# Kernel optimization log

Hardware: AMD Instinct MI355X
Metric: run time of the kernel (lower is better)

Reference implementation:

```python
import jax, jax.numpy as jnp
import numpy as np

M0, M1 = 32, 16          # multiplicities of 0e (scalars) and 1o (vectors)
FEAT = M0 + 3 * M1       # 80
WNUM = M0*M0 + M1*M1 + M0*M1 + M1*M0  # 2304 per-edge TP weights
N_NODES, N_EDGES, N_RBF, HID = 10000, 160000, 50, 64
EPS = 1e-5
INV_SQRT3 = 1.0 / np.sqrt(3.0)
# per-path normalization: 1/sqrt(num_paths_to_output * mul_in)
A_P1 = 1.0 / np.sqrt(2.0 * M0)   # 0e x 0e -> 0e
A_P4 = 1.0 / np.sqrt(2.0 * M1)   # 1o x 1o -> 0e
A_P2 = 1.0 / np.sqrt(2.0 * M1)   # 1o x 0e -> 1o
A_P3 = 1.0 / np.sqrt(2.0 * M0)   # 0e x 1o -> 1o


def setup_inputs() -> dict:
    key = jax.random.key(0)
    ks = jax.random.split(key, 12)
    def lin(k, fi, fo):
        return jax.random.normal(k, (fi, fo), jnp.float32) / np.sqrt(fi)
    return dict(
        h=jax.random.normal(ks[0], (N_NODES, FEAT), jnp.float32),
        edge_index=jax.random.randint(ks[1], (2, N_EDGES), 0, N_NODES),
        edge_sh=jax.random.normal(ks[2], (N_EDGES, 4), jnp.float32),
        edge_features=jax.random.normal(ks[3], (N_EDGES, N_RBF), jnp.float32),
        W1e=lin(ks[4], N_RBF, HID), b1e=jnp.zeros(HID, jnp.float32),
        W2e=lin(ks[5], HID, HID), b2e=jnp.zeros(HID, jnp.float32),
        W3e=lin(ks[6], HID, WNUM) * 0.1, b3e=jnp.zeros(WNUM, jnp.float32),
        A0=jax.random.normal(ks[7], (M0, M0), jnp.float32),
        A1p=jax.random.normal(ks[8], (M1, M1), jnp.float32),
        bn_w0=jnp.ones(M0, jnp.float32), bn_b0=jnp.zeros(M0, jnp.float32),
        bn_w1=jnp.ones(M1, jnp.float32),
    )


def _forward(h, edge_index, edge_sh, edge_features,
             W1e, b1e, W2e, b2e, W3e, b3e, A0, A1p, bn_w0, bn_b0, bn_w1):
    N = h.shape[0]
    E = edge_sh.shape[0]
    src, dst = edge_index[0], edge_index[1]

    # ---- edge MLP -> per-edge tensor-product weights [E, WNUM] ----
    w = jax.nn.silu(edge_features @ W1e + b1e)
    w = jax.nn.silu(w @ W2e + b2e)
    w = w @ W3e + b3e
    o1 = M0 * M0
    o2 = o1 + M1 * M1
    o3 = o2 + M0 * M1
    w1 = w[:, :o1].reshape(E, M0, M0)     # 0e x 0e -> 0e
    w2 = w[:, o1:o2].reshape(E, M1, M1)   # 1o x 0e -> 1o
    w3 = w[:, o2:o3].reshape(E, M0, M1)   # 0e x 1o -> 1o
    w4 = w[:, o3:].reshape(E, M1, M0)     # 1o x 1o -> 0e

    # ---- gather source node features ----
    s0 = h[src, :M0]                         # [E, M0]
    s1 = h[src, M0:].reshape(E, M1, 3)       # [E, M1, 3]
    y0 = edge_sh[:, 0]                       # [E]
    y1 = edge_sh[:, 1:4]                     # [E, 3]

    # ---- fully connected tensor product with per-edge weights ----
    # scalar output: 0e x 0e -> 0e  and  1o x 1o -> 0e (dot / sqrt(3))
    dot11 = jnp.einsum('eui,ei->eu', s1, y1) * INV_SQRT3      # [E, M1]
    m0 = (A_P1 * jnp.einsum('eu,euw->ew', s0 * y0[:, None], w1)
          + A_P4 * jnp.einsum('eu,euw->ew', dot11, w4))       # [E, M0]
    # vector output: 1o x 0e -> 1o  and  0e x 1o -> 1o
    m1 = (A_P2 * jnp.einsum('eui,euw->ewi', s1 * y0[:, None, None], w2)
          + A_P3 * jnp.einsum('eu,ei,euw->ewi', s0, y1, w3))  # [E, M1, 3]
    messages = jnp.concatenate([m0, m1.reshape(E, 3 * M1)], axis=1)  # [E, FEAT]

    # ---- scatter-mean aggregation to destination nodes ----
    agg = jax.ops.segment_sum(messages, dst, num_segments=N)
    cnt = jax.ops.segment_sum(jnp.ones((E,), messages.dtype), dst, num_segments=N)
    agg = agg / jnp.maximum(cnt, 1.0)[:, None]

    # ---- equivariant self-interaction (per-l linear mixing) ----
    self0 = (h[:, :M0] @ A0) / np.sqrt(M0)
    h1 = h[:, M0:].reshape(N, M1, 3)
    self1 = jnp.einsum('nui,uw->nwi', h1, A1p) / np.sqrt(M1)
    out = agg + jnp.concatenate([self0, self1.reshape(N, 3 * M1)], axis=1)

    # ---- equivariant batch norm (layer mode) ----
    x0 = out[:, :M0]
    x1 = out[:, M0:].reshape(N, M1, 3)
    mu = x0.mean(axis=0)
    var = x0.var(axis=0)
    x0n = (x0 - mu) * jax.lax.rsqrt(var + EPS) * bn_w0 + bn_b0
    nrm2 = (x1 ** 2).sum(axis=-1).mean(axis=0)               # [M1]
    x1n = x1 * (jax.lax.rsqrt(nrm2 + EPS) * bn_w1)[None, :, None]
    out = jnp.concatenate([x0n, x1n.reshape(N, 3 * M1)], axis=1)

    # ---- residual (irreps_in == irreps_out) ----
    return out + h


def reference(h, edge_index, edge_sh, edge_features,
              W1e, b1e, W2e, b2e, W3e, b3e, A0, A1p, bn_w0, bn_b0, bn_w1):
    return _forward(h, edge_index, edge_sh, edge_features,
                    W1e, b1e, W2e, b2e, W3e, b3e, A0, A1p, bn_w0, bn_b0, bn_w1)
```

## Files before the change

### kernel.cpp

```cpp
#include <hip/hip_runtime.h>
#include <math.h>

#define NN 10000
#define NE 160000
#define NRBF 50
#define WNUM 2304
#define EPSV 1e-5f

#define A_P1 0.125f
#define A_P2 0.17677669529663687f
#define A_P3 0.125f
#define A_P4 0.17677669529663687f
#define INV_SQRT3 0.5773502691896258f
#define INV_SQRT_M0 0.17677669529663687f
#define INV_SQRT_M1 0.25f

typedef __attribute__((ext_vector_type(8))) short bf16x8;
typedef __attribute__((ext_vector_type(4))) float f32x4;
typedef __attribute__((ext_vector_type(4))) int i32x4;

#define MFMA16(a, b, c) __builtin_amdgcn_mfma_f32_16x16x32_bf16(a, b, c, 0, 0, 0)

__device__ __forceinline__ short f2bf(float x) {
  unsigned u = __float_as_uint(x);
  unsigned r = (u + 0x7fffu + ((u >> 16) & 1u)) >> 16;
  return (short)r;
}

__global__ void prep_weights(const float* __restrict__ W1, const float* __restrict__ W2,
                             const float* __restrict__ W3, short* __restrict__ W1P,
                             short* __restrict__ W2P, short* __restrict__ W3P) {
  int s = blockIdx.x * 256 + threadIdx.x;
  if (s < WNUM * 64) {
    int t = s >> 10, r = s & 1023;
    int ch = r >> 9, l = (r >> 3) & 63, kk = r & 7;
    int row = t * 16 + (l & 15);
    int k = ((l >> 4) << 3) + (ch << 5) + kk;
    W3P[s] = f2bf(W3[k * WNUM + row]);
  } else if (s < WNUM * 64 + 4096) {
    int s2 = s - WNUM * 64;
    int t = s2 >> 10, r = s2 & 1023;
    int ch = r >> 9, l = (r >> 3) & 63, kk = r & 7;
    int row = t * 16 + (l & 15);
    int k = ((l >> 4) << 3) + (ch << 5) + kk;
    W1P[s2] = f2bf(k < NRBF ? W1[k * 64 + row] : 0.f);
  } else if (s < WNUM * 64 + 8192) {
    int s2 = s - WNUM * 64 - 4096;
    int t = s2 >> 10, r = s2 & 1023;
    int ch = r >> 9, l = (r >> 3) & 63, kk = r & 7;
    int row = t * 16 + (l & 15);
    int k = ((l >> 4) << 3) + (ch << 5) + kk;
    W2P[s2] = f2bf(W2[k * 64 + row]);
  }
}

__global__ __launch_bounds__(256, 3) void edge_kernel(
    const float* __restrict__ h, const int* __restrict__ eidx,
    const float* __restrict__ esh, const float* __restrict__ ef,
    const short* __restrict__ W1P, const float* __restrict__ b1,
    const short* __restrict__ W2P, const float* __restrict__ b2,
    const short* __restrict__ W3P, const float* __restrict__ b3,
    float* __restrict__ agg, float* __restrict__ cnt) {
  __shared__ short act[64 * 72];
  __shared__ float coef[6144];
  __shared__ float y0s[64], y1s[192];
  __shared__ float b1s[64], b2s[64];
  __shared__ int dsts[64];
  float* scratch = coef;

  const int tid = threadIdx.x;
  const int e0 = blockIdx.x * 64;

  for (int idx = tid; idx < 64 * 64; idx += 256) {
    int e = idx >> 6, k = idx & 63;
    float v = (k < NRBF) ? ef[(long)(e0 + e) * NRBF + k] : 0.f;
    act[e * 72 + k] = f2bf(v);
  }
  if (tid < 64) { b1s[tid] = b1[tid]; b2s[tid] = b2[tid]; }
  {
    int e = tid >> 2, q = tid & 3;
    int ge = e0 + e;
    int src = eidx[ge];
    float y0 = esh[ge * 4 + 0];
    float y1x = esh[ge * 4 + 1], y1y = esh[ge * 4 + 2], y1z = esh[ge * 4 + 3];
    const float* hs = h + (long)src * 80;
    for (int u = q; u < 32; u += 4) coef[u * 64 + e] = 0.125f * hs[u];
    for (int u = q; u < 16; u += 4) {
      float sx = hs[32 + u * 3], sy = hs[33 + u * 3], sz = hs[34 + u * 3];
      coef[2048 + u * 64 + e] = A_P2 * sx;
      coef[3072 + u * 64 + e] = A_P2 * sy;
      coef[4096 + u * 64 + e] = A_P2 * sz;
      coef[5120 + u * 64 + e] = A_P4 * INV_SQRT3 * (sx * y1x + sy * y1y + sz * y1z);
    }
    if (q == 0) {
      y0s[e] = y0;
      y1s[e] = y1x; y1s[64 + e] = y1y; y1s[128 + e] = y1z;
      dsts[e] = eidx[NE + ge];
    }
  }
  __syncthreads();

  const int wid = tid >> 6, l = tid & 63;
  const int lr = l & 15, lg = l >> 4;
  const int g16 = lg * 4;
  const int er = wid * 16;

  {
    bf16x8 a0 = *(const bf16x8*)&act[(er + lr) * 72 + lg * 8];
    bf16x8 a1 = *(const bf16x8*)&act[(er + lr) * 72 + 32 + lg * 8];
#pragma unroll
    for (int jt = 0; jt < 4; ++jt) {
      const short* wb = W1P + (jt << 10) + (l << 3);
      bf16x8 b0 = *(const bf16x8*)wb;
      bf16x8 b1f = *(const bf16x8*)(wb + 512);
      float bias = b1s[jt * 16 + lr];
      f32x4 d = {bias, bias, bias, bias};
      d = MFMA16(a0, b0, d);
      d = MFMA16(a1, b1f, d);
#pragma unroll
      for (int r = 0; r < 4; ++r) {
        float x = d[r];
        x = x / (1.f + __expf(-x));
        act[(er + lg * 4 + r) * 72 + jt * 16 + lr] = f2bf(x);
      }
    }
  }
  {
    bf16x8 a0 = *(const bf16x8*)&act[(er + lr) * 72 + lg * 8];
    bf16x8 a1 = *(const bf16x8*)&act[(er + lr) * 72 + 32 + lg * 8];
#pragma unroll
    for (int jt = 0; jt < 4; ++jt) {
      const short* wb = W2P + (jt << 10) + (l << 3);
      bf16x8 b0 = *(const bf16x8*)wb;
      bf16x8 b1f = *(const bf16x8*)(wb + 512);
      float bias = b2s[jt * 16 + lr];
      f32x4 d = {bias, bias, bias, bias};
      d = MFMA16(a0, b0, d);
      d = MFMA16(a1, b1f, d);
#pragma unroll
      for (int r = 0; r < 4; ++r) {
        float x = d[r];
        x = x / (1.f + __expf(-x));
        act[(er + lg * 4 + r) * 72 + jt * 16 + lr] = f2bf(x);
      }
    }
  }
  __syncthreads();

  bf16x8 a0g[4], a1g[4];
#pragma unroll
  for (int g = 0; g < 4; ++g) {
    a0g[g] = *(const bf16x8*)&act[(g * 16 + lr) * 72 + lg * 8];
    a1g[g] = *(const bf16x8*)&act[(g * 16 + lr) * 72 + 32 + lg * 8];
  }

#define M0_PAIR(TE, COFF)                                            \
  {                                                                  \
    const short* wbE = W3P + ((TE) << 10) + (l << 3);                \
    const short* wbO = W3P + (((TE) + 1) << 10) + (l << 3);          \
    bf16x8 E0 = *(const bf16x8*)wbE;                                 \
    bf16x8 E1 = *(const bf16x8*)(wbE + 512);                         \
    bf16x8 O0 = *(const bf16x8*)wbO;                                 \
    bf16x8 O1 = *(const bf16x8*)(wbO + 512);                         \
    float be = b3[((TE) << 4) + lr];                                 \
    float bo = b3[(((TE) + 1) << 4) + lr];                           \
    _Pragma("unroll")                                                \
    for (int g = 0; g < 4; ++g) {                                    \
      f32x4 c = *(const f32x4*)&coef[(COFF) + g * 16 + g16];         \
      f32x4 d = {be, be, be, be};                                    \
      d = MFMA16(a0g[g], E0, d);                                     \
      f32x4 v = MFMA16(a1g[g], E1, d);                               \
      f32x4 d2 = {bo, bo, bo, bo};                                   \
      d2 = MFMA16(a0g[g], O0, d2);                                   \
      f32x4 v2 = MFMA16(a1g[g], O1, d2);                             \
      _Pragma("unroll")                                              \
      for (int r = 0; r < 4; ++r) {                                  \
        acc0[g][r] += c[r] * v[r];                                   \
        acc1[g][r] += c[r] * v2[r];                                  \
      }                                                              \
    }                                                                \
  }

#define W2_TILE(U)                                                   \
  {                                                                  \
    const short* wb = W3P + ((64 + (U)) << 10) + (l << 3);           \
    bf16x8 B0 = *(const bf16x8*)wb;                                  \
    bf16x8 B1 = *(const bf16x8*)(wb + 512);                          \
    float bb = b3[((64 + (U)) << 4) + lr];                           \
    _Pragma("unroll")                                                \
    for (int g = 0; g < 4; ++g) {                                    \
      f32x4 d = {bb, bb, bb, bb};                                    \
      d = MFMA16(a0g[g], B0, d);                                     \
      f32x4 v = MFMA16(a1g[g], B1, d);                               \
      f32x4 cx = *(const f32x4*)&coef[2048 + (U) * 64 + g * 16 + g16]; \
      f32x4 cy = *(const f32x4*)&coef[3072 + (U) * 64 + g * 16 + g16]; \
      f32x4 cz = *(const f32x4*)&coef[4096 + (U) * 64 + g * 16 + g16]; \
      _Pragma("unroll")                                              \
      for (int r = 0; r < 4; ++r) {                                  \
        mx[g][r] += cx[r] * v[r];                                    \
        my[g][r] += cy[r] * v[r];                                    \
        mz[g][r] += cz[r] * v[r];                                    \
      }                                                              \
    }                                                                \
  }

#define W3_TILE(U)                                                   \
  {                                                                  \
    const short* wb = W3P + ((80 + (U)) << 10) + (l << 3);           \
    bf16x8 B0 = *(const bf16x8*)wb;                                  \
    bf16x8 B1 = *(const bf16x8*)(wb + 512);                          \
    float bb = b3[((80 + (U)) << 4) + lr];                           \
    _Pragma("unroll")                                                \
    for (int g = 0; g < 4; ++g) {                                    \
      f32x4 d = {bb, bb, bb, bb};                                    \
      d = MFMA16(a0g[g], B0, d);                                     \
      f32x4 v = MFMA16(a1g[g], B1, d);                               \
      f32x4 c = *(const f32x4*)&coef[(U) * 64 + g * 16 + g16];       \
      _Pragma("unroll")                                              \
      for (int r = 0; r < 4; ++r) t3[g][r] += c[r] * v[r];           \
    }                                                                \
  }

  if (wid < 2) {
    f32x4 acc0[4], acc1[4];
#pragma unroll
    for (int g = 0; g < 4; ++g) {
      acc0[g] = (f32x4){0, 0, 0, 0};
      acc1[g] = (f32x4){0, 0, 0, 0};
    }
    if (wid == 0) {
#pragma unroll 2
      for (int u = 0; u < 24; ++u) M0_PAIR(2 * u, u * 64);
#pragma unroll
      for (int g = 0; g < 4; ++g) {
        f32x4 y0v = *(const f32x4*)&y0s[g * 16 + g16];
#pragma unroll
        for (int r = 0; r < 4; ++r) { acc0[g][r] *= y0v[r]; acc1[g][r] *= y0v[r]; }
      }
    } else {
#pragma unroll 2
      for (int u = 24; u < 32; ++u) M0_PAIR(2 * u, u * 64);
#pragma unroll
      for (int g = 0; g < 4; ++g) {
        f32x4 y0v = *(const f32x4*)&y0s[g * 16 + g16];
#pragma unroll
        for (int r = 0; r < 4; ++r) { acc0[g][r] *= y0v[r]; acc1[g][r] *= y0v[r]; }
      }
#pragma unroll 2
      for (int p = 0; p < 16; ++p) M0_PAIR(112 + 2 * p, 5120 + p * 64);
    }
    __syncthreads();
    if (wid == 1) {
      float* p = scratch + l * 20;
      *(f32x4*)(p + 0) = acc0[0]; *(f32x4*)(p + 4) = acc1[0];
      *(f32x4*)(p + 8) = acc0[1]; *(f32x4*)(p + 12) = acc1[1];
    } else {
      float* p = scratch + 1280 + l * 20;
      *(f32x4*)(p + 0) = acc0[2]; *(f32x4*)(p + 4) = acc1[2];
      *(f32x4*)(p + 8) = acc0[3]; *(f32x4*)(p + 12) = acc1[3];
    }
    __syncthreads();
    const int gb = (wid == 0) ? 0 : 2;
    const float* p = (wid == 0) ? (scratch + l * 20) : (scratch + 1280 + l * 20);
    f32x4 t0 = *(const f32x4*)(p + 0), t1 = *(const f32x4*)(p + 4);
    f32x4 t2 = *(const f32x4*)(p + 8), t3_ = *(const f32x4*)(p + 12);
    i32x4 dd0 = *(const i32x4*)&dsts[(gb + 0) * 16 + g16];
    i32x4 dd1 = *(const i32x4*)&dsts[(gb + 1) * 16 + g16];
#pragma unroll
    for (int r = 0; r < 4; ++r) {
      float* base = agg + (long)dd0[r] * 80;
      atomicAdd(base + lr, acc0[gb + 0][r] + t0[r]);
      atomicAdd(base + 16 + lr, acc1[gb + 0][r] + t1[r]);
    }
#pragma unroll
    for (int r = 0; r < 4; ++r) {
      float* base = agg + (long)dd1[r] * 80;
      atomicAdd(base + lr, acc0[gb + 1][r] + t2[r]);
      atomicAdd(base + 16 + lr, acc1[gb + 1][r] + t3_[r]);
    }
  } else {
    f32x4 mx[4], my[4], mz[4], t3[4];
#pragma unroll
    for (int g = 0; g < 4; ++g) {
      mx[g] = (f32x4){0, 0, 0, 0}; my[g] = (f32x4){0, 0, 0, 0};
      mz[g] = (f32x4){0, 0, 0, 0}; t3[g] = (f32x4){0, 0, 0, 0};
    }
    if (wid == 2) {
#pragma unroll 2
      for (int u = 0; u < 8; ++u) W2_TILE(u);
#pragma unroll 2
      for (int u = 0; u < 16; ++u) W3_TILE(u);
    } else {
#pragma unroll 2
      for (int u = 8; u < 16; ++u) W2_TILE(u);
#pragma unroll 2
      for (int u = 16; u < 32; ++u) W3_TILE(u);
    }
#pragma unroll
    for (int g = 0; g < 4; ++g) {
      f32x4 y0v = *(const f32x4*)&y0s[g * 16 + g16];
      f32x4 yx = *(const f32x4*)&y1s[g * 16 + g16];
      f32x4 yy = *(const f32x4*)&y1s[64 + g * 16 + g16];
      f32x4 yz = *(const f32x4*)&y1s[128 + g * 16 + g16];
#pragma unroll
      for (int r = 0; r < 4; ++r) {
        mx[g][r] = mx[g][r] * y0v[r] + yx[r] * t3[g][r];
        my[g][r] = my[g][r] * y0v[r] + yy[r] * t3[g][r];
        mz[g][r] = mz[g][r] * y0v[r] + yz[r] * t3[g][r];
      }
    }
    __syncthreads();
    if (wid == 3) {
      float* p = scratch + 2560 + l * 28;
      *(f32x4*)(p + 0) = mx[0]; *(f32x4*)(p + 4) = my[0]; *(f32x4*)(p + 8) = mz[0];
      *(f32x4*)(p + 12) = mx[1]; *(f32x4*)(p + 16) = my[1]; *(f32x4*)(p + 20) = mz[1];
    } else {
      float* p = scratch + 4352 + l * 28;
      *(f32x4*)(p + 0) = mx[2]; *(f32x4*)(p + 4) = my[2]; *(f32x4*)(p + 8) = mz[2];
      *(f32x4*)(p + 12) = mx[3]; *(f32x4*)(p + 16) = my[3]; *(f32x4*)(p + 20) = mz[3];
    }
    __syncthreads();
    const int gb = (wid == 2) ? 0 : 2;
    const float* p = (wid == 2) ? (scratch + 2560 + l * 28) : (scratch + 4352 + l * 28);
    f32x4 u0 = *(const f32x4*)(p + 0), u1 = *(const f32x4*)(p + 4);
    f32x4 u2 = *(const f32x4*)(p + 8), u3 = *(const f32x4*)(p + 12);
    f32x4 u4 = *(const f32x4*)(p + 16), u5 = *(const f32x4*)(p + 20);
    i32x4 dd0 = *(const i32x4*)&dsts[(gb + 0) * 16 + g16];
    i32x4 dd1 = *(const i32x4*)&dsts[(gb + 1) * 16 + g16];
#pragma unroll
    for (int r = 0; r < 4; ++r) {
      float* base = agg + (long)dd0[r] * 80;
      atomicAdd(base + 32 + lr * 3 + 0, mx[gb + 0][r] + u0[r]);
      atomicAdd(base + 32 + lr * 3 + 1, my[gb + 0][r] + u1[r]);
      atomicAdd(base + 32 + lr * 3 + 2, mz[gb + 0][r] + u2[r]);
    }
#pragma unroll
    for (int r = 0; r < 4; ++r) {
      float* base = agg + (long)dd1[r] * 80;
      atomicAdd(base + 32 + lr * 3 + 0, mx[gb + 1][r] + u3[r]);
      atomicAdd(base + 32 + lr * 3 + 1, my[gb + 1][r] + u4[r]);
      atomicAdd(base + 32 + lr * 3 + 2, mz[gb + 1][r] + u5[r]);
    }
  }
  if (tid < 64) atomicAdd(cnt + dsts[tid], 1.0f);
#undef M0_PAIR
#undef W2_TILE
#undef W3_TILE
}

__global__ __launch_bounds__(256) void node_a(
    const float* __restrict__ h, const float* __restrict__ A0,
    const float* __restrict__ A1p, const float* __restrict__ agg,
    const float* __restrict__ cnt, float* __restrict__ outpre,
    float* __restrict__ stats) {
  __shared__ float A0s[1024], A1ps[256], red[80];
  const int tid = threadIdx.x;
  for (int i = tid; i < 1280; i += 256) {
    if (i < 1024) A0s[i] = A0[i];
    else A1ps[i - 1024] = A1p[i - 1024];
  }
  if (tid < 80) red[tid] = 0.f;
  __syncthreads();
  const int wid = tid >> 6, l = tid & 63;

  float s1 = 0.f, s2 = 0.f, s3 = 0.f;

  const int jA = l - 32;
  const int wA = (l >= 32) ? jA / 3 : 0;
  const int iA = (l >= 32) ? jA - wA * 3 : 0;
  const int jB = 32 + l;
  const int wB = jB / 3;
  const int iB = jB - wB * 3;

#pragma unroll 1
  for (int it = 0; it < 4; ++it) {
    const int n = blockIdx.x * 16 + wid * 4 + it;
    const float* hr = h + (long)n * 80;
    const float* ar = agg + (long)n * 80;
    const float inv = 1.f / fmaxf(cnt[n], 1.f);
    float valA;
    if (l < 32) {
      float x = 0.f;
#pragma unroll 8
      for (int u = 0; u < 32; ++u) x += hr[u] * A0s[u * 32 + l];
      valA = x * INV_SQRT_M0 + ar[l] * inv;
    } else {
      float x = 0.f;
#pragma unroll 8
      for (int u = 0; u < 16; ++u) x += hr[32 + u * 3 + iA] * A1ps[u * 16 + wA];
      valA = x * INV_SQRT_M1 + ar[l] * inv;
    }
    float valB = 0.f;
    if (l < 16) {
      float x = 0.f;
#pragma unroll 8
      for (int u = 0; u < 16; ++u) x += hr[32 + u * 3 + iB] * A1ps[u * 16 + wB];
      valB = x * INV_SQRT_M1 + ar[64 + l] * inv;
    }
    outpre[(long)n * 80 + l] = valA;
    if (l < 16) outpre[(long)n * 80 + 64 + l] = valB;
    if (l < 32) { s1 += valA; s2 += valA * valA; }
    else s2 += valA * valA;
    if (l < 16) s3 += valB * valB;
  }

  if (l < 32) {
    atomicAdd(&red[l], s1);
    atomicAdd(&red[32 + l], s2);
  } else {
    atomicAdd(&red[64 + wA], s2);
  }
  if (l < 16) atomicAdd(&red[64 + wB], s3);
  __syncthreads();
  if (tid < 80) atomicAdd(&stats[tid], red[tid]);
}

__global__ void node_b(const float* __restrict__ outpre, const float* __restrict__ stats,
                       const float* __restrict__ bnw0, const float* __restrict__ bnb0,
                       const float* __restrict__ bnw1, const float* __restrict__ h,
                       float* __restrict__ out) {
  int idx = blockIdx.x * 256 + threadIdx.x;
  if (idx >= NN * 80) return;
  int c = idx % 80;
  float v = outpre[idx];
  const float invN = 1.f / NN;
  float o;
  if (c < 32) {
    float mu = stats[c] * invN;
    float var = stats[32 + c] * invN - mu * mu;
    o = (v - mu) * rsqrtf(var + EPSV) * bnw0[c] + bnb0[c];
  } else {
    int u = (c - 32) / 3;
    float nr = stats[64 + u] * invN;
    o = v * rsqrtf(nr + EPSV) * bnw1[u];
  }
  out[idx] = o + h[idx];
}

extern "C" void kernel_launch(void* const* d_in, const int* in_sizes, int n_in,
                              void* d_out, int out_size, void* d_ws, size_t ws_size,
                              hipStream_t stream) {
  const float* h    = (const float*)d_in[0];
  const int*   eidx = (const int*)d_in[1];
  const float* esh  = (const float*)d_in[2];
  const float* ef   = (const float*)d_in[3];
  const float* W1   = (const float*)d_in[4];
  const float* b1   = (const float*)d_in[5];
  const float* W2   = (const float*)d_in[6];
  const float* b2   = (const float*)d_in[7];
  const float* W3   = (const float*)d_in[8];
  const float* b3   = (const float*)d_in[9];
  const float* A0   = (const float*)d_in[10];
  const float* A1p  = (const float*)d_in[11];
  const float* bnw0 = (const float*)d_in[12];
  const float* bnb0 = (const float*)d_in[13];
  const float* bnw1 = (const float*)d_in[14];
  float* out = (float*)d_out;

  float* ws = (float*)d_ws;
  float* agg    = ws;
  float* cnt    = ws + 800000;
  float* stats  = ws + 810000;
  float* outpre = ws + 810080;
  short* W3P    = (short*)(ws + 1610080);
  short* W1P    = W3P + WNUM * 64;
  short* W2P    = W1P + 4096;

  hipMemsetAsync(agg, 0, (size_t)810080 * sizeof(float), stream);

  prep_weights<<<(WNUM * 64 + 8192 + 255) / 256, 256, 0, stream>>>(W1, W2, W3, W1P,
                                                                   W2P, W3P);
  edge_kernel<<<NE / 64, 256, 0, stream>>>(h, eidx, esh, ef, W1P, b1, W2P, b2, W3P, b3,
                                           agg, cnt);
  node_a<<<NN / 16, 256, 0, stream>>>(h, A0, A1p, agg, cnt, outpre, stats);
  node_b<<<(NN * 80 + 255) / 256, 256, 0, stream>>>(outpre, stats, bnw0, bnb0, bnw1, h,
                                                    out);
}
```

Baseline: 204.2 us.

## Split edge kernel into separate MLP and tensor-product fold kernels

The first two edge-MLP layers move into their own kernel, which writes the bf16 hidden activations to a global buffer. The fold kernel then reads those activations straight from global memory instead of LDS. This drops the act buffer's shared memory from the heavy kernel and may raise occupancy or ease register pressure. In exchange it adds an extra launch and a 20 MB global round trip for the hidden activations.

```diff
diff --git a/kernel.cpp b/kernel.cpp
--- a/kernel.cpp
+++ b/kernel.cpp
@@ -54,20 +54,12 @@
   }
 }
 
-__global__ __launch_bounds__(256, 3) void edge_kernel(
-    const float* __restrict__ h, const int* __restrict__ eidx,
-    const float* __restrict__ esh, const float* __restrict__ ef,
-    const short* __restrict__ W1P, const float* __restrict__ b1,
-    const short* __restrict__ W2P, const float* __restrict__ b2,
-    const short* __restrict__ W3P, const float* __restrict__ b3,
-    float* __restrict__ agg, float* __restrict__ cnt) {
+__global__ __launch_bounds__(256) void edge_mlp(
+    const float* __restrict__ ef, const short* __restrict__ W1P,
+    const float* __restrict__ b1, const short* __restrict__ W2P,
+    const float* __restrict__ b2, short* __restrict__ h2buf) {
   __shared__ short act[64 * 72];
-  __shared__ float coef[6144];
-  __shared__ float y0s[64], y1s[192];
   __shared__ float b1s[64], b2s[64];
-  __shared__ int dsts[64];
-  float* scratch = coef;
-
   const int tid = threadIdx.x;
   const int e0 = blockIdx.x * 64;
 
@@ -77,6 +69,73 @@
     act[e * 72 + k] = f2bf(v);
   }
   if (tid < 64) { b1s[tid] = b1[tid]; b2s[tid] = b2[tid]; }
+  __syncthreads();
+
+  const int wid = tid >> 6, l = tid & 63;
+  const int lr = l & 15, lg = l >> 4;
+  const int er = wid * 16;
+
+  {
+    bf16x8 a0 = *(const bf16x8*)&act[(er + lr) * 72 + lg * 8];
+    bf16x8 a1 = *(const bf16x8*)&act[(er + lr) * 72 + 32 + lg * 8];
+#pragma unroll
+    for (int jt = 0; jt < 4; ++jt) {
+      const short* wb = W1P + (jt << 10) + (l << 3);
+      bf16x8 b0 = *(const bf16x8*)wb;
+      bf16x8 b1f = *(const bf16x8*)(wb + 512);
+      float bias = b1s[jt * 16 + lr];
+      f32x4 d = {bias, bias, bias, bias};
+      d = MFMA16(a0, b0, d);
+      d = MFMA16(a1, b1f, d);
+#pragma unroll
+      for (int r = 0; r < 4; ++r) {
+        float x = d[r];
+        x = x / (1.f + __expf(-x));
+        act[(er + lg * 4 + r) * 72 + jt * 16 + lr] = f2bf(x);
+      }
+    }
+  }
+  {
+    bf16x8 a0 = *(const bf16x8*)&act[(er + lr) * 72 + lg * 8];
+    bf16x8 a1 = *(const bf16x8*)&act[(er + lr) * 72 + 32 + lg * 8];
+#pragma unroll
+    for (int jt = 0; jt < 4; ++jt) {
+      const short* wb = W2P + (jt << 10) + (l << 3);
+      bf16x8 b0 = *(const bf16x8*)wb;
+      bf16x8 b1f = *(const bf16x8*)(wb + 512);
+      float bias = b2s[jt * 16 + lr];
+      f32x4 d = {bias, bias, bias, bias};
+      d = MFMA16(a0, b0, d);
+      d = MFMA16(a1, b1f, d);
+#pragma unroll
+      for (int r = 0; r < 4; ++r) {
+        float x = d[r];
+        x = x / (1.f + __expf(-x));
+        act[(er + lg * 4 + r) * 72 + jt * 16 + lr] = f2bf(x);
+      }
+    }
+  }
+#pragma unroll
+  for (int i = l; i < 128; i += 64) {
+    int row = er + (i >> 3), c4 = i & 7;
+    *(i32x4*)(h2buf + (long)(e0 + row) * 64 + c4 * 8) =
+        *(const i32x4*)&act[row * 72 + c4 * 8];
+  }
+}
+
+__global__ __launch_bounds__(256, 3) void edge_fold(
+    const float* __restrict__ h, const int* __restrict__ eidx,
+    const float* __restrict__ esh, const short* __restrict__ h2buf,
+    const short* __restrict__ W3P, const float* __restrict__ b3,
+    float* __restrict__ agg, float* __restrict__ cnt) {
+  __shared__ float coef[6144];
+  __shared__ float y0s[64], y1s[192];
+  __shared__ int dsts[64];
+  float* scratch = coef;
+
+  const int tid = threadIdx.x;
+  const int e0 = blockIdx.x * 64;
+
   {
     int e = tid >> 2, q = tid & 3;
     int ge = e0 + e;
@@ -103,55 +162,13 @@
   const int wid = tid >> 6, l = tid & 63;
   const int lr = l & 15, lg = l >> 4;
   const int g16 = lg * 4;
-  const int er = wid * 16;
-
-  {
-    bf16x8 a0 = *(const bf16x8*)&act[(er + lr) * 72 + lg * 8];
-    bf16x8 a1 = *(const bf16x8*)&act[(er + lr) * 72 + 32 + lg * 8];
-#pragma unroll
-    for (int jt = 0; jt < 4; ++jt) {
-      const short* wb = W1P + (jt << 10) + (l << 3);
-      bf16x8 b0 = *(const bf16x8*)wb;
-      bf16x8 b1f = *(const bf16x8*)(wb + 512);
-      float bias = b1s[jt * 16 + lr];
-      f32x4 d = {bias, bias, bias, bias};
-      d = MFMA16(a0, b0, d);
-      d = MFMA16(a1, b1f, d);
-#pragma unroll
-      for (int r = 0; r < 4; ++r) {
-        float x = d[r];
-        x = x / (1.f + __expf(-x));
-        act[(er + lg * 4 + r) * 72 + jt * 16 + lr] = f2bf(x);
-      }
-    }
-  }
-  {
-    bf16x8 a0 = *(const bf16x8*)&act[(er + lr) * 72 + lg * 8];
-    bf16x8 a1 = *(const bf16x8*)&act[(er + lr) * 72 + 32 + lg * 8];
-#pragma unroll
-    for (int jt = 0; jt < 4; ++jt) {
-      const short* wb = W2P + (jt << 10) + (l << 3);
-      bf16x8 b0 = *(const bf16x8*)wb;
-      bf16x8 b1f = *(const bf16x8*)(wb + 512);
-      float bias = b2s[jt * 16 + lr];
-      f32x4 d = {bias, bias, bias, bias};
-      d = MFMA16(a0, b0, d);
-      d = MFMA16(a1, b1f, d);
-#pragma unroll
-      for (int r = 0; r < 4; ++r) {
-        float x = d[r];
-        x = x / (1.f + __expf(-x));
-        act[(er + lg * 4 + r) * 72 + jt * 16 + lr] = f2bf(x);
-      }
-    }
-  }
-  __syncthreads();
 
   bf16x8 a0g[4], a1g[4];
 #pragma unroll
   for (int g = 0; g < 4; ++g) {
-    a0g[g] = *(const bf16x8*)&act[(g * 16 + lr) * 72 + lg * 8];
-    a1g[g] = *(const bf16x8*)&act[(g * 16 + lr) * 72 + 32 + lg * 8];
+    const short* hp = h2buf + (long)(e0 + g * 16 + lr) * 64;
+    a0g[g] = *(const bf16x8*)(hp + lg * 8);
+    a1g[g] = *(const bf16x8*)(hp + 32 + lg * 8);
   }
 
 #define M0_PAIR(TE, COFF)                                            \
@@ -465,13 +482,14 @@
   short* W3P    = (short*)(ws + 1610080);
   short* W1P    = W3P + WNUM * 64;
   short* W2P    = W1P + 4096;
+  short* h2buf  = W2P + 4096;
 
   hipMemsetAsync(agg, 0, (size_t)810080 * sizeof(float), stream);
 
   prep_weights<<<(WNUM * 64 + 8192 + 255) / 256, 256, 0, stream>>>(W1, W2, W3, W1P,
                                                                    W2P, W3P);
-  edge_kernel<<<NE / 64, 256, 0, stream>>>(h, eidx, esh, ef, W1P, b1, W2P, b2, W3P, b3,
-                                           agg, cnt);
+  edge_mlp<<<NE / 64, 256, 0, stream>>>(ef, W1P, b1, W2P, b2, h2buf);
+  edge_fold<<<NE / 64, 256, 0, stream>>>(h, eidx, esh, h2buf, W3P, b3, agg, cnt);
   node_a<<<NN / 16, 256, 0, stream>>>(h, A0, A1p, agg, cnt, outpre, stats);
   node_b<<<(NN * 80 + 255) / 256, 256, 0, stream>>>(outpre, stats, bnw0, bnb0, bnw1, h,
                                                     out);
```

New measurement: 211.6 us. 1.04x slower.
